# Kernel optimization log

Hardware: AMD Instinct MI355X
Metric: run time of the kernel (lower is better)

Reference implementation:

```python
import jax, jax.numpy as jnp
import numpy as np

B, T, C, K = 8, 2048, 1024, 128

def setup_inputs() -> dict:
    key = jax.random.key(0)
    k1, k2, k3, k4 = jax.random.split(key, 4)
    scale = 0.02
    return {
        "x": jax.random.normal(k1, (B, T, C), dtype=jnp.float32),
        "Wq": jax.random.normal(k2, (C, K), dtype=jnp.float32) * scale,
        "Wk": jax.random.normal(k3, (C, K), dtype=jnp.float32) * scale,
        "Wv": jax.random.normal(k4, (C, K), dtype=jnp.float32) * scale,
    }

def reference(x, Wq, Wk, Wv):
    # Single-head causal self-attention (ModulUwagi.forward)
    q = jnp.einsum('btc,ck->btk', x, Wq)  # [B,T,K]
    k = jnp.einsum('btc,ck->btk', x, Wk)
    v = jnp.einsum('btc,ck->btk', x, Wv)
    hd = q.shape[-1]
    wei = jnp.einsum('btk,bsk->bts', q, k) * (hd ** -0.5)  # [B,T,T]
    causal = jnp.tril(jnp.ones((x.shape[1], x.shape[1]), dtype=bool))
    wei = jnp.where(causal, wei, -jnp.inf)
    wei = jax.nn.softmax(wei, axis=-1)
    out = jnp.einsum('bts,bsk->btk', wei, v)  # [B,T,K]
    return out
```

## Files before the change

kernel.cpp:

```cpp
#include <hip/hip_runtime.h>
#include <cmath>

#define Bn 8
#define Tn 2048
#define Cn 1024
#define Kn 128

typedef __attribute__((ext_vector_type(8))) short short8;
typedef __attribute__((ext_vector_type(4))) float f32x4;
typedef unsigned short u16;
typedef unsigned int u32;

#define NEGINF (-__builtin_huge_valf())

__device__ __forceinline__ u16 f2b(float f) {
    u32 u = __float_as_uint(f);
    u32 r = (u + 0x7FFFu + ((u >> 16) & 1u)) >> 16;
    return (u16)r;
}
__device__ __forceinline__ float b2f(u16 v) {
    u32 u = ((u32)v) << 16;
    return __uint_as_float(u);
}
__device__ __forceinline__ u32 cvtpk(float lo, float hi) {
    u32 r;
    asm("v_cvt_pk_bf16_f32 %0, %1, %2" : "=v"(r) : "v"(lo), "v"(hi));
    return r;
}

__device__ __forceinline__ void load_lds16(const u16* g, u16* l) {
    __builtin_amdgcn_global_load_lds(
        (const __attribute__((address_space(1))) u32*)(g),
        (__attribute__((address_space(3))) u32*)(l), 16, 0, 0);
}

__global__ __launch_bounds__(256)
void prep_kernel(const float* __restrict__ Wq, const float* __restrict__ Wk,
                 const float* __restrict__ Wv, u16* __restrict__ Wt)
{
    int id = blockIdx.x * 256 + threadIdx.x;
    int w   = id >> 15;
    int rem = id & 32767;
    int c   = rem >> 5;
    int n4  = (rem & 31) << 2;
    const float* W = (w == 0) ? Wq : (w == 1) ? Wk : Wv;
    float4 v = *(const float4*)(W + (size_t)c * Kn + n4);
    u16* dst = Wt + (size_t)w * Kn * Cn;
    dst[(size_t)(n4 + 0) * Cn + c] = f2b(v.x);
    dst[(size_t)(n4 + 1) * Cn + c] = f2b(v.y);
    dst[(size_t)(n4 + 2) * Cn + c] = f2b(v.z);
    dst[(size_t)(n4 + 3) * Cn + c] = f2b(v.w);
}

__global__ __launch_bounds__(256)
void proj5_kernel(const float* __restrict__ x, const u16* __restrict__ Wt,
                  u16* __restrict__ qkv)
{
    const int bid = blockIdx.x;
    const int g8  = bid >> 3, xr = bid & 7;
    const int w   = g8 % 3;
    const int rt  = (g8 / 3) * 8 + xr;
    const u16* wtg = Wt + (size_t)w * Kn * Cn;
    u16* outp = qkv + (size_t)w * Bn * Tn * Kn;
    const int row0 = rt * 64;
    const int tid  = threadIdx.x;
    const int lane = tid & 63;
    const int wid  = tid >> 6;
    const int l15  = lane & 15, lh = lane >> 4;
    const int m0 = (wid >> 1) * 32, n0 = (wid & 1) * 64;

    __shared__ u16 lds[24576];

    auto stageW = [&](int kk, int buf) {
        #pragma unroll
        for (int i = 0; i < 4; ++i) {
            int u = tid + i * 256;
            int n = u >> 3, c8 = u & 7;
            load_lds16(wtg + (size_t)n * Cn + kk + ((c8 ^ (n & 7)) << 3),
                       lds + 8192 + buf * 8192 + u * 8);
        }
    };
    auto loadX = [&](int kk, float4* xr4) {
        #pragma unroll
        for (int i = 0; i < 2; ++i) {
            int u = tid + i * 256;
            int r = u >> 3, c8 = u & 7;
            const float* s = x + (size_t)(row0 + r) * Cn + kk + c8 * 8;
            xr4[2 * i]     = *(const float4*)(s);
            xr4[2 * i + 1] = *(const float4*)(s + 4);
        }
    };
    auto writeX = [&](int buf, const float4* xr4) {
        u16* dst = lds + buf * 4096;
        #pragma unroll
        for (int i = 0; i < 2; ++i) {
            int u = tid + i * 256;
            int r = u >> 3, c8 = u & 7;
            uint4 pk;
            pk.x = cvtpk(xr4[2 * i].x,     xr4[2 * i].y);
            pk.y = cvtpk(xr4[2 * i].z,     xr4[2 * i].w);
            pk.z = cvtpk(xr4[2 * i + 1].x, xr4[2 * i + 1].y);
            pk.w = cvtpk(xr4[2 * i + 1].z, xr4[2 * i + 1].w);
            *(uint4*)(dst + r * 64 + ((c8 ^ (r & 7)) << 3)) = pk;
        }
    };

    f32x4 acc[2][4];
    #pragma unroll
    for (int i = 0; i < 2; ++i)
        #pragma unroll
        for (int j = 0; j < 4; ++j) acc[i][j] = (f32x4){0.f, 0.f, 0.f, 0.f};

    auto compute = [&](int buf) {
        const u16* Xb = lds + buf * 4096;
        const u16* Wb = lds + 8192 + buf * 8192;
        #pragma unroll
        for (int kc = 0; kc < 2; ++kc) {
            short8 af[2], bf[4];
            #pragma unroll
            for (int mg = 0; mg < 2; ++mg) {
                int row = m0 + mg * 16 + l15;
                int ch  = (kc * 4 + lh) ^ (row & 7);
                af[mg] = *(const short8*)(Xb + row * 64 + ch * 8);
            }
            #pragma unroll
            for (int ng = 0; ng < 4; ++ng) {
                int n  = n0 + ng * 16 + l15;
                int ch = (kc * 4 + lh) ^ (n & 7);
                bf[ng] = *(const short8*)(Wb + n * 64 + ch * 8);
            }
            #pragma unroll
            for (int mg = 0; mg < 2; ++mg)
                #pragma unroll
                for (int ng = 0; ng < 4; ++ng)
                    acc[mg][ng] = __builtin_amdgcn_mfma_f32_16x16x32_bf16(
                        af[mg], bf[ng], acc[mg][ng], 0, 0, 0);
        }
    };

    float4 xA[4], xB[4];
    loadX(0, xA);
    stageW(0, 0);
    loadX(64, xB);
    writeX(0, xA);
    asm volatile("s_waitcnt vmcnt(4) lgkmcnt(0)" ::: "memory");
    __builtin_amdgcn_sched_barrier(0);
    __builtin_amdgcn_s_barrier();
    __builtin_amdgcn_sched_barrier(0);

    auto step = [&](int t, float4* XW, float4* XL) {
        const int buf = t & 1;
        if (t + 1 < 16) stageW((t + 1) * 64, buf ^ 1);
        if (t + 2 < 16) loadX((t + 2) * 64, XL);
        compute(buf);
        if (t + 1 < 16) writeX(buf ^ 1, XW);
        if (t < 15) {
            if (t < 14)
                asm volatile("s_waitcnt vmcnt(4) lgkmcnt(0)" ::: "memory");
            else
                asm volatile("s_waitcnt vmcnt(0) lgkmcnt(0)" ::: "memory");
            __builtin_amdgcn_sched_barrier(0);
            __builtin_amdgcn_s_barrier();
            __builtin_amdgcn_sched_barrier(0);
        }
    };

    for (int tt = 0; tt < 8; ++tt) {
        step(2 * tt,     xB, xA);
        step(2 * tt + 1, xA, xB);
    }

    #pragma unroll
    for (int mg = 0; mg < 2; ++mg)
        #pragma unroll
        for (int ng = 0; ng < 4; ++ng)
            #pragma unroll
            for (int r = 0; r < 4; ++r) {
                int m = row0 + m0 + mg * 16 + lh * 4 + r;
                int n = n0 + ng * 16 + l15;
                outp[(size_t)m * Kn + n] = f2b(acc[mg][ng][r]);
            }
}

__device__ const int g_job_qi[32] = {0, 1,1, 2,2,2, 3,3,3,3, 4,4,4,4,
                                     5,5,5,5,5, 6,6,6,6,6,6, 7,7,7,7,7,7,7};
__device__ const int g_sup_b[32] = {0, 0,4, 0,4,8, 0,4,8,12, 0,5,10,15,
                                    0,4,9,14,19, 0,4,9,14,18,23, 0,4,9,13,18,22,27};
__device__ const int g_sup_e[32] = {4, 4,8, 4,8,12, 4,8,12,16, 5,10,15,20,
                                    4,9,14,19,24, 4,9,14,18,23,28, 4,9,13,18,22,27,32};

__global__ __launch_bounds__(512, 2)
void attn_kernel(const u16* __restrict__ qg_, const u16* __restrict__ kg_,
                 const u16* __restrict__ vg_, u16* __restrict__ pO,
                 float* __restrict__ pM, float* __restrict__ pL)
{
    const int b   = blockIdx.x;
    const int job = blockIdx.y;
    const int qi  = g_job_qi[job];
    const int sb  = g_sup_b[job], se = g_sup_e[job];

    const u16* qw = qg_ + (size_t)b * Tn * Kn;
    const u16* kw = kg_ + (size_t)b * Tn * Kn;
    const u16* vw = vg_ + (size_t)b * Tn * Kn;

    const int tid  = threadIdx.x;
    const int lane = tid & 63;
    const int wid  = tid >> 6;
    const int l15  = lane & 15, lh = lane >> 4;

    const int q0 = qi * 256 + wid * 32;
    const int qmax_w = q0 + 31;

    __shared__ u16 lds[32768];

    short8 qf[2][4];
    #pragma unroll
    for (int g = 0; g < 2; ++g)
        #pragma unroll
        for (int kc = 0; kc < 4; ++kc)
            qf[g][kc] = *(const short8*)(qw + (size_t)(q0 + g * 16 + l15) * Kn
                                         + kc * 32 + lh * 8);

    f32x4 acc[8][2];
    #pragma unroll
    for (int dt = 0; dt < 8; ++dt)
        #pragma unroll
        for (int g = 0; g < 2; ++g) acc[dt][g] = (f32x4){0.f, 0.f, 0.f, 0.f};
    float m_g[2] = {NEGINF, NEGINF}, l_g[2] = {0.f, 0.f};

    const float scale = 0.08838834764831843f;

    auto stageK = [&](int sup, int buf) {
        const u16* src = kw + (size_t)sup * 64 * Kn;
        u16* dst = lds + buf * 8192;
        #pragma unroll
        for (int i = 0; i < 2; ++i) {
            int u = wid * 128 + i * 64 + lane;
            int row = u >> 4;
            int c16 = (u & 15) ^ (row & 7);
            load_lds16(src + (size_t)row * Kn + c16 * 8,
                       dst + (size_t)(wid * 128 + i * 64) * 8);
        }
    };
    auto loadV = [&](int sup, uint4* vr) {
        const u16* src = vw + (size_t)sup * 64 * Kn;
        #pragma unroll
        for (int r = 0; r < 2; ++r) {
            int s  = tid & 63;
            int u8 = (tid >> 6) + 8 * r;
            vr[r] = *(const uint4*)(src + (size_t)s * Kn + u8 * 8);
        }
    };
    auto writeV = [&](int buf, const uint4* vr) {
        u16* dst = lds + 16384 + buf * 8192;
        #pragma unroll
        for (int r = 0; r < 2; ++r) {
            int s  = tid & 63;
            int u8 = (tid >> 6) + 8 * r;
            const u16* e = (const u16*)&vr[r];
            #pragma unroll
            for (int j = 0; j < 8; ++j) {
                int d = u8 * 8 + j;
                dst[d * 64 + (((s >> 3) ^ j) << 3) + (s & 7)] = e[j];
            }
        }
    };

    uint4 vreg[2];
    stageK(sb, 0);
    loadV(sb, vreg);
    writeV(0, vreg);

    for (int sup = sb; sup < se; ++sup) {
        const int cur = (sup - sb) & 1;
        __syncthreads();
        const bool have_next = (sup + 1 < se);
        if (have_next) {
            stageK(sup + 1, cur ^ 1);
            loadV(sup + 1, vreg);
        }
        if (sup * 64 <= qmax_w) {
            const u16* Kb = lds + cur * 8192;
            const u16* Vb = lds + 16384 + cur * 8192;
            f32x4 sf[4][2];
            #pragma unroll
            for (int mt = 0; mt < 4; ++mt)
                #pragma unroll
                for (int g = 0; g < 2; ++g) sf[mt][g] = (f32x4){0.f,0.f,0.f,0.f};
            #pragma unroll
            for (int kc = 0; kc < 4; ++kc) {
                short8 a[4];
                #pragma unroll
                for (int mt = 0; mt < 4; ++mt) {
                    int row = mt * 16 + l15;
                    int ch  = (kc * 4 + lh) ^ (row & 7);
                    a[mt] = *(const short8*)(Kb + row * 128 + ch * 8);
                }
                #pragma unroll
                for (int mt = 0; mt < 4; ++mt)
                    #pragma unroll
                    for (int g = 0; g < 2; ++g)
                        sf[mt][g] = __builtin_amdgcn_mfma_f32_16x16x32_bf16(
                            a[mt], qf[g][kc], sf[mt][g], 0, 0, 0);
            }
            const int sbase = sup * 64;
            u32 upk[2][4][2];
            float alpha_g[2];
            #pragma unroll
            for (int g = 0; g < 2; ++g) {
                const int qg = q0 + g * 16 + l15;
                float pv[16];
                float pm = NEGINF;
                #pragma unroll
                for (int mt = 0; mt < 4; ++mt)
                    #pragma unroll
                    for (int r = 0; r < 4; ++r) {
                        int sg = sbase + mt * 16 + lh * 4 + r;
                        float vv = sf[mt][g][r] * scale;
                        vv = (sg > qg) ? NEGINF : vv;
                        pv[mt * 4 + r] = vv;
                        pm = fmaxf(pm, vv);
                    }
                pm = fmaxf(pm, __shfl_xor(pm, 16));
                pm = fmaxf(pm, __shfl_xor(pm, 32));
                float mn  = fmaxf(m_g[g], pm);
                float mns = (mn == NEGINF) ? 0.f : mn;
                float al  = __expf(m_g[g] - mns);
                m_g[g] = mn;
                alpha_g[g] = al;
                float ps = 0.f;
                #pragma unroll
                for (int i = 0; i < 16; ++i) { pv[i] = __expf(pv[i] - mns); ps += pv[i]; }
                ps += __shfl_xor(ps, 16);
                ps += __shfl_xor(ps, 32);
                l_g[g] = l_g[g] * al + ps;
                #pragma unroll
                for (int mt = 0; mt < 4; ++mt)
                    #pragma unroll
                    for (int h = 0; h < 2; ++h)
                        upk[g][mt][h] = (u32)f2b(pv[mt * 4 + 2 * h])
                                      | ((u32)f2b(pv[mt * 4 + 2 * h + 1]) << 16);
            }
            #pragma unroll
            for (int dt = 0; dt < 8; ++dt)
                #pragma unroll
                for (int g = 0; g < 2; ++g)
                    acc[dt][g] *= alpha_g[g];
            #pragma unroll
            for (int ks = 0; ks < 2; ++ks) {
                short8 pf[2];
                #pragma unroll
                for (int g = 0; g < 2; ++g) {
                    union { u32 w[4]; short8 v; } uu;
                    #pragma unroll
                    for (int hp = 0; hp < 4; ++hp) {
                        int srcLane = l15 + 16 * ((lh & 1) * 2 + (hp >> 1));
                        u32 vA = __shfl(upk[g][2 * ks][hp & 1], srcLane, 64);
                        u32 vB = __shfl(upk[g][2 * ks + 1][hp & 1], srcLane, 64);
                        uu.w[hp] = (lh < 2) ? vA : vB;
                    }
                    pf[g] = uu.v;
                }
                #pragma unroll
                for (int dt = 0; dt < 8; ++dt) {
                    int d  = dt * 16 + l15;
                    int ch = (ks * 4 + lh) ^ (d & 7);
                    short8 av = *(const short8*)(Vb + d * 64 + ch * 8);
                    #pragma unroll
                    for (int g = 0; g < 2; ++g)
                        acc[dt][g] = __builtin_amdgcn_mfma_f32_16x16x32_bf16(
                            av, pf[g], acc[dt][g], 0, 0, 0);
                }
            }
        }
        if (have_next) writeV(cur ^ 1, vreg);
    }

    const size_t slotrow = ((size_t)b * 32 + job) * 256 + wid * 32;
    #pragma unroll
    for (int g = 0; g < 2; ++g) {
        size_t row = slotrow + g * 16 + l15;
        #pragma unroll
        for (int dt = 0; dt < 8; ++dt) {
            ushort4 o = { f2b(acc[dt][g][0]), f2b(acc[dt][g][1]),
                          f2b(acc[dt][g][2]), f2b(acc[dt][g][3]) };
            *(ushort4*)(pO + row * 128 + dt * 16 + lh * 4) = o;
        }
        if (lh == 0) {
            pM[row] = m_g[g];
            pL[row] = l_g[g];
        }
    }
}

__device__ const int g_cnt[8] = {1, 2, 3, 4, 4, 5, 6, 7};
__device__ const int g_s0[8]  = {0, 1, 3, 6, 10, 14, 19, 25};

__global__ __launch_bounds__(256)
void merge_kernel(const u16* __restrict__ pO, const float* __restrict__ pM,
                  const float* __restrict__ pL, float* __restrict__ out)
{
    const int bid = blockIdx.x;
    const int b   = bid >> 8;
    const int rem = bid & 255;
    const int qi  = rem >> 5;
    const int rg  = rem & 31;
    const int c = g_cnt[qi], s0 = g_s0[qi];
    const int tid = threadIdx.x;
    const int r8 = tid >> 5;
    const int dg = tid & 31;

    const int row = rg * 8 + r8;
    const size_t base = ((size_t)b * 32 + s0) * 256 + row;

    float mv[8];
    float M = NEGINF;
    #pragma unroll
    for (int i = 0; i < 8; ++i)
        if (i < c) { mv[i] = pM[base + (size_t)i * 256]; M = fmaxf(M, mv[i]); }
    float L = 0.f, w[8];
    #pragma unroll
    for (int i = 0; i < 8; ++i)
        if (i < c) {
            float e = __expf(mv[i] - M);
            L += pL[base + (size_t)i * 256] * e;
            w[i] = e;
        }
    const float invL = 1.f / L;

    float4 o = {0.f, 0.f, 0.f, 0.f};
    #pragma unroll
    for (int i = 0; i < 8; ++i)
        if (i < c) {
            ushort4 p = *(const ushort4*)(pO + (base + (size_t)i * 256) * 128 + dg * 4);
            float wi = w[i] * invL;
            o.x = fmaf(wi, b2f(p.x), o.x);
            o.y = fmaf(wi, b2f(p.y), o.y);
            o.z = fmaf(wi, b2f(p.z), o.z);
            o.w = fmaf(wi, b2f(p.w), o.w);
        }
    *(float4*)(out + ((size_t)b * Tn + qi * 256 + row) * Kn + dg * 4) = o;
}

extern "C" void kernel_launch(void* const* d_in, const int* in_sizes, int n_in,
                              void* d_out, int out_size, void* d_ws, size_t ws_size,
                              hipStream_t stream)
{
    const float* x  = (const float*)d_in[0];
    const float* Wq = (const float*)d_in[1];
    const float* Wk = (const float*)d_in[2];
    const float* Wv = (const float*)d_in[3];
    float* out = (float*)d_out;

    u16* ws = (u16*)d_ws;
    const size_t btk = (size_t)Bn * Tn * Kn;
    u16* q  = ws;
    u16* k  = ws + btk;
    u16* v  = ws + 2 * btk;
    u16* Wt = ws + 3 * btk;
    u16* pO = ws + 3 * btk + 393216;
    float* pM = (float*)(pO + (size_t)8388608);
    float* pL = pM + 65536;

    prep_kernel<<<384, 256, 0, stream>>>(Wq, Wk, Wv, Wt);
    proj5_kernel<<<768, 256, 0, stream>>>(x, Wt, ws);
    attn_kernel<<<dim3(Bn, 32), 512, 0, stream>>>(q, k, v, pO, pM, pL);
    merge_kernel<<<2048, 256, 0, stream>>>(pO, pM, pL, out);
}
```

Measured before the change: 67.08 us.

## Halve attention query tile to 128 rows and split into 72 balanced jobs

Attention blocks now cover 128 query rows with 4 waves (256 threads) instead of 256 rows with 8 waves, and the KV range is split into 72 jobs per batch instead of 32. The staging loops are reworked so fewer threads still fill the same K/V LDS tiles, and the merge kernel and workspace offsets are resized to match. The aim is finer load balance and more blocks across CUs. In exchange, each K/V tile is reused by fewer query rows, and there are more partial outputs to write and merge.

```diff
diff --git a/kernel.cpp b/kernel.cpp
--- a/kernel.cpp
+++ b/kernel.cpp
@@ -12,6 +12,7 @@
 typedef unsigned int u32;
 
 #define NEGINF (-__builtin_huge_valf())
+#define NJOBS 72
 
 __device__ __forceinline__ u16 f2b(float f) {
     u32 u = __float_as_uint(f);
@@ -182,14 +183,23 @@
             }
 }
 
-__device__ const int g_job_qi[32] = {0, 1,1, 2,2,2, 3,3,3,3, 4,4,4,4,
-                                     5,5,5,5,5, 6,6,6,6,6,6, 7,7,7,7,7,7,7};
-__device__ const int g_sup_b[32] = {0, 0,4, 0,4,8, 0,4,8,12, 0,5,10,15,
-                                    0,4,9,14,19, 0,4,9,14,18,23, 0,4,9,13,18,22,27};
-__device__ const int g_sup_e[32] = {4, 4,8, 4,8,12, 4,8,12,16, 5,10,15,20,
-                                    4,9,14,19,24, 4,9,14,18,23,28, 4,9,13,18,22,27,32};
-
-__global__ __launch_bounds__(512, 2)
+__device__ const int g_job_qi[NJOBS] = {
+    0, 1, 2,2, 3,3, 4,4,4, 5,5,5, 6,6,6,6, 7,7,7,7,
+    8,8,8,8,8, 9,9,9,9,9, 10,10,10,10,10,10, 11,11,11,11,11,11,
+    12,12,12,12,12,12,12, 13,13,13,13,13,13,13,
+    14,14,14,14,14,14,14,14, 15,15,15,15,15,15,15,15};
+__device__ const int g_sup_b[NJOBS] = {
+    0, 0, 0,3, 0,4, 0,4,7, 0,4,8, 0,4,8,11, 0,4,8,12,
+    0,4,8,12,15, 0,4,8,12,16, 0,4,8,12,16,19, 0,4,8,12,16,20,
+    0,4,8,12,16,20,23, 0,4,8,12,16,20,24,
+    0,4,8,12,16,20,24,27, 0,4,8,12,16,20,24,28};
+__device__ const int g_sup_e[NJOBS] = {
+    2, 4, 3,6, 4,8, 4,7,10, 4,8,12, 4,8,11,14, 4,8,12,16,
+    4,8,12,15,18, 4,8,12,16,20, 4,8,12,16,19,22, 4,8,12,16,20,24,
+    4,8,12,16,20,23,26, 4,8,12,16,20,24,28,
+    4,8,12,16,20,24,27,30, 4,8,12,16,20,24,28,32};
+
+__global__ __launch_bounds__(256, 2)
 void attn_kernel(const u16* __restrict__ qg_, const u16* __restrict__ kg_,
                  const u16* __restrict__ vg_, u16* __restrict__ pO,
                  float* __restrict__ pM, float* __restrict__ pL)
@@ -208,7 +218,7 @@
     const int wid  = tid >> 6;
     const int l15  = lane & 15, lh = lane >> 4;
 
-    const int q0 = qi * 256 + wid * 32;
+    const int q0 = qi * 128 + wid * 32;
     const int qmax_w = q0 + 31;
 
     __shared__ u16 lds[32768];
@@ -234,29 +244,30 @@
         const u16* src = kw + (size_t)sup * 64 * Kn;
         u16* dst = lds + buf * 8192;
         #pragma unroll
-        for (int i = 0; i < 2; ++i) {
-            int u = wid * 128 + i * 64 + lane;
+        for (int i = 0; i < 4; ++i) {
+            int base = wid * 256 + i * 64;
+            int u = base + lane;
             int row = u >> 4;
             int c16 = (u & 15) ^ (row & 7);
             load_lds16(src + (size_t)row * Kn + c16 * 8,
-                       dst + (size_t)(wid * 128 + i * 64) * 8);
+                       dst + (size_t)base * 8);
         }
     };
     auto loadV = [&](int sup, uint4* vr) {
         const u16* src = vw + (size_t)sup * 64 * Kn;
         #pragma unroll
-        for (int r = 0; r < 2; ++r) {
+        for (int r = 0; r < 4; ++r) {
             int s  = tid & 63;
-            int u8 = (tid >> 6) + 8 * r;
+            int u8 = (tid >> 6) + 4 * r;
             vr[r] = *(const uint4*)(src + (size_t)s * Kn + u8 * 8);
         }
     };
     auto writeV = [&](int buf, const uint4* vr) {
         u16* dst = lds + 16384 + buf * 8192;
         #pragma unroll
-        for (int r = 0; r < 2; ++r) {
+        for (int r = 0; r < 4; ++r) {
             int s  = tid & 63;
-            int u8 = (tid >> 6) + 8 * r;
+            int u8 = (tid >> 6) + 4 * r;
             const u16* e = (const u16*)&vr[r];
             #pragma unroll
             for (int j = 0; j < 8; ++j) {
@@ -266,7 +277,7 @@
         }
     };
 
-    uint4 vreg[2];
+    uint4 vreg[4];
     stageK(sb, 0);
     loadV(sb, vreg);
     writeV(0, vreg);
@@ -376,7 +387,7 @@
         if (have_next) writeV(cur ^ 1, vreg);
     }
 
-    const size_t slotrow = ((size_t)b * 32 + job) * 256 + wid * 32;
+    const size_t slotrow = ((size_t)b * NJOBS + job) * 128 + wid * 32;
     #pragma unroll
     for (int g = 0; g < 2; ++g) {
         size_t row = slotrow + g * 16 + l15;
@@ -393,8 +404,8 @@
     }
 }
 
-__device__ const int g_cnt[8] = {1, 2, 3, 4, 4, 5, 6, 7};
-__device__ const int g_s0[8]  = {0, 1, 3, 6, 10, 14, 19, 25};
+__device__ const int g_cnt[16] = {1,1,2,2,3,3,4,4,5,5,6,6,7,7,8,8};
+__device__ const int g_s0[16]  = {0,1,2,4,6,9,12,16,20,25,30,36,42,49,56,64};
 
 __global__ __launch_bounds__(256)
 void merge_kernel(const u16* __restrict__ pO, const float* __restrict__ pM,
@@ -403,27 +414,27 @@
     const int bid = blockIdx.x;
     const int b   = bid >> 8;
     const int rem = bid & 255;
-    const int qi  = rem >> 5;
-    const int rg  = rem & 31;
+    const int qi  = rem >> 4;
+    const int rg  = rem & 15;
     const int c = g_cnt[qi], s0 = g_s0[qi];
     const int tid = threadIdx.x;
     const int r8 = tid >> 5;
     const int dg = tid & 31;
 
     const int row = rg * 8 + r8;
-    const size_t base = ((size_t)b * 32 + s0) * 256 + row;
+    const size_t base = ((size_t)b * NJOBS + s0) * 128 + row;
 
     float mv[8];
     float M = NEGINF;
     #pragma unroll
     for (int i = 0; i < 8; ++i)
-        if (i < c) { mv[i] = pM[base + (size_t)i * 256]; M = fmaxf(M, mv[i]); }
+        if (i < c) { mv[i] = pM[base + (size_t)i * 128]; M = fmaxf(M, mv[i]); }
     float L = 0.f, w[8];
     #pragma unroll
     for (int i = 0; i < 8; ++i)
         if (i < c) {
             float e = __expf(mv[i] - M);
-            L += pL[base + (size_t)i * 256] * e;
+            L += pL[base + (size_t)i * 128] * e;
             w[i] = e;
         }
     const float invL = 1.f / L;
@@ -432,14 +443,14 @@
     #pragma unroll
     for (int i = 0; i < 8; ++i)
         if (i < c) {
-            ushort4 p = *(const ushort4*)(pO + (base + (size_t)i * 256) * 128 + dg * 4);
+            ushort4 p = *(const ushort4*)(pO + (base + (size_t)i * 128) * 128 + dg * 4);
             float wi = w[i] * invL;
             o.x = fmaf(wi, b2f(p.x), o.x);
             o.y = fmaf(wi, b2f(p.y), o.y);
             o.z = fmaf(wi, b2f(p.z), o.z);
             o.w = fmaf(wi, b2f(p.w), o.w);
         }
-    *(float4*)(out + ((size_t)b * Tn + qi * 256 + row) * Kn + dg * 4) = o;
+    *(float4*)(out + ((size_t)b * Tn + qi * 128 + row) * Kn + dg * 4) = o;
 }
 
 extern "C" void kernel_launch(void* const* d_in, const int* in_sizes, int n_in,
@@ -459,11 +470,11 @@
     u16* v  = ws + 2 * btk;
     u16* Wt = ws + 3 * btk;
     u16* pO = ws + 3 * btk + 393216;
-    float* pM = (float*)(pO + (size_t)8388608);
-    float* pL = pM + 65536;
+    float* pM = (float*)(pO + (size_t)9437184);
+    float* pL = pM + 73728;
 
     prep_kernel<<<384, 256, 0, stream>>>(Wq, Wk, Wv, Wt);
     proj5_kernel<<<768, 256, 0, stream>>>(x, Wt, ws);
-    attn_kernel<<<dim3(Bn, 32), 512, 0, stream>>>(q, k, v, pO, pM, pL);
+    attn_kernel<<<dim3(Bn, NJOBS), 256, 0, stream>>>(q, k, v, pO, pM, pL);
     merge_kernel<<<2048, 256, 0, stream>>>(pO, pM, pL, out);
 }
```

Measured after the change: 78.04 us. +16.3%, slower.

## Fuse QKV projections into one block per row tile, load weights directly to registers

Applied to the files above, without the earlier changes.

The projection kernel now computes all three Q/K/V outputs (384 columns) for a 64-row tile in a single 512-thread block, so each x tile is read from global memory and converted to bf16 once instead of three times. Weight fragments are loaded straight from global memory into registers with double buffering, skipping the LDS staging of W. This cuts x traffic roughly threefold and reduces LDS use. The cost is higher register pressure (24 short8 weight fragments per thread), uncoalesced-ish per-lane weight reads that rely on L2, and fewer blocks (256) to spread across the CUs.

```diff
diff --git a/kernel.cpp b/kernel.cpp
--- a/kernel.cpp
+++ b/kernel.cpp
@@ -52,113 +52,94 @@
     dst[(size_t)(n4 + 3) * Cn + c] = f2b(v.w);
 }
 
-__global__ __launch_bounds__(256)
-void proj5_kernel(const float* __restrict__ x, const u16* __restrict__ Wt,
+__global__ __launch_bounds__(512, 2)
+void proj6_kernel(const float* __restrict__ x, const u16* __restrict__ Wt,
                   u16* __restrict__ qkv)
 {
-    const int bid = blockIdx.x;
-    const int g8  = bid >> 3, xr = bid & 7;
-    const int w   = g8 % 3;
-    const int rt  = (g8 / 3) * 8 + xr;
-    const u16* wtg = Wt + (size_t)w * Kn * Cn;
-    u16* outp = qkv + (size_t)w * Bn * Tn * Kn;
+    const int rt   = blockIdx.x;
     const int row0 = rt * 64;
     const int tid  = threadIdx.x;
     const int lane = tid & 63;
     const int wid  = tid >> 6;
     const int l15  = lane & 15, lh = lane >> 4;
-    const int m0 = (wid >> 1) * 32, n0 = (wid & 1) * 64;
-
-    __shared__ u16 lds[24576];
-
-    auto stageW = [&](int kk, int buf) {
-        #pragma unroll
-        for (int i = 0; i < 4; ++i) {
-            int u = tid + i * 256;
-            int n = u >> 3, c8 = u & 7;
-            load_lds16(wtg + (size_t)n * Cn + kk + ((c8 ^ (n & 7)) << 3),
-                       lds + 8192 + buf * 8192 + u * 8);
-        }
-    };
-    auto loadX = [&](int kk, float4* xr4) {
-        #pragma unroll
-        for (int i = 0; i < 2; ++i) {
-            int u = tid + i * 256;
-            int r = u >> 3, c8 = u & 7;
-            const float* s = x + (size_t)(row0 + r) * Cn + kk + c8 * 8;
-            xr4[2 * i]     = *(const float4*)(s);
-            xr4[2 * i + 1] = *(const float4*)(s + 4);
-        }
-    };
-    auto writeX = [&](int buf, const float4* xr4) {
-        u16* dst = lds + buf * 4096;
-        #pragma unroll
-        for (int i = 0; i < 2; ++i) {
-            int u = tid + i * 256;
-            int r = u >> 3, c8 = u & 7;
-            uint4 pk;
-            pk.x = cvtpk(xr4[2 * i].x,     xr4[2 * i].y);
-            pk.y = cvtpk(xr4[2 * i].z,     xr4[2 * i].w);
-            pk.z = cvtpk(xr4[2 * i + 1].x, xr4[2 * i + 1].y);
-            pk.w = cvtpk(xr4[2 * i + 1].z, xr4[2 * i + 1].w);
-            *(uint4*)(dst + r * 64 + ((c8 ^ (r & 7)) << 3)) = pk;
-        }
-    };
-
-    f32x4 acc[2][4];
+    const int wm0 = (wid >> 2) * 32;
+    const int wn0 = (wid & 3) * 96;
+
+    __shared__ u16 xs[8192];
+
+    const u16* wb[6];
+    #pragma unroll
+    for (int ng = 0; ng < 6; ++ng)
+        wb[ng] = Wt + (size_t)(wn0 + ng * 16 + l15) * Cn + lh * 8;
+
+    auto loadW = [&](int kk, short8* wf) {
+        #pragma unroll
+        for (int kc = 0; kc < 2; ++kc)
+            #pragma unroll
+            for (int ng = 0; ng < 6; ++ng)
+                wf[kc * 6 + ng] = *(const short8*)(wb[ng] + kk + kc * 32);
+    };
+    auto loadX = [&](int kk, float4* xr) {
+        int r = tid >> 3, c8 = tid & 7;
+        const float* s = x + (size_t)(row0 + r) * Cn + kk + c8 * 8;
+        xr[0] = *(const float4*)(s);
+        xr[1] = *(const float4*)(s + 4);
+    };
+    auto writeX = [&](int buf, const float4* xr) {
+        int r = tid >> 3, c8 = tid & 7;
+        uint4 pk;
+        pk.x = cvtpk(xr[0].x, xr[0].y);
+        pk.y = cvtpk(xr[0].z, xr[0].w);
+        pk.z = cvtpk(xr[1].x, xr[1].y);
+        pk.w = cvtpk(xr[1].z, xr[1].w);
+        *(uint4*)(xs + buf * 4096 + r * 64 + ((c8 ^ (r & 7)) << 3)) = pk;
+    };
+
+    f32x4 acc[2][6];
     #pragma unroll
     for (int i = 0; i < 2; ++i)
         #pragma unroll
-        for (int j = 0; j < 4; ++j) acc[i][j] = (f32x4){0.f, 0.f, 0.f, 0.f};
-
-    auto compute = [&](int buf) {
-        const u16* Xb = lds + buf * 4096;
-        const u16* Wb = lds + 8192 + buf * 8192;
+        for (int j = 0; j < 6; ++j) acc[i][j] = (f32x4){0.f, 0.f, 0.f, 0.f};
+
+    auto compute = [&](int buf, const short8* wf) {
+        const u16* Xb = xs + buf * 4096;
         #pragma unroll
         for (int kc = 0; kc < 2; ++kc) {
-            short8 af[2], bf[4];
+            short8 af[2];
             #pragma unroll
             for (int mg = 0; mg < 2; ++mg) {
-                int row = m0 + mg * 16 + l15;
+                int row = wm0 + mg * 16 + l15;
                 int ch  = (kc * 4 + lh) ^ (row & 7);
                 af[mg] = *(const short8*)(Xb + row * 64 + ch * 8);
             }
             #pragma unroll
-            for (int ng = 0; ng < 4; ++ng) {
-                int n  = n0 + ng * 16 + l15;
-                int ch = (kc * 4 + lh) ^ (n & 7);
-                bf[ng] = *(const short8*)(Wb + n * 64 + ch * 8);
-            }
-            #pragma unroll
             for (int mg = 0; mg < 2; ++mg)
                 #pragma unroll
-                for (int ng = 0; ng < 4; ++ng)
+                for (int ng = 0; ng < 6; ++ng)
                     acc[mg][ng] = __builtin_amdgcn_mfma_f32_16x16x32_bf16(
-                        af[mg], bf[ng], acc[mg][ng], 0, 0, 0);
-        }
-    };
-
-    float4 xA[4], xB[4];
+                        af[mg], wf[kc * 6 + ng], acc[mg][ng], 0, 0, 0);
+        }
+    };
+
+    short8 wfA[12], wfB[12];
+    float4 xA[2], xB[2];
     loadX(0, xA);
-    stageW(0, 0);
+    loadW(0, wfA);
     loadX(64, xB);
     writeX(0, xA);
-    asm volatile("s_waitcnt vmcnt(4) lgkmcnt(0)" ::: "memory");
+    asm volatile("s_waitcnt lgkmcnt(0)" ::: "memory");
     __builtin_amdgcn_sched_barrier(0);
     __builtin_amdgcn_s_barrier();
     __builtin_amdgcn_sched_barrier(0);
 
-    auto step = [&](int t, float4* XW, float4* XL) {
+    auto step = [&](int t, float4* xW, float4* xL, short8* wfCur, short8* wfNext) {
         const int buf = t & 1;
-        if (t + 1 < 16) stageW((t + 1) * 64, buf ^ 1);
-        if (t + 2 < 16) loadX((t + 2) * 64, XL);
-        compute(buf);
-        if (t + 1 < 16) writeX(buf ^ 1, XW);
+        if (t + 2 < 16) loadX((t + 2) * 64, xL);
+        if (t + 1 < 16) loadW((t + 1) * 64, wfNext);
+        compute(buf, wfCur);
+        if (t + 1 < 16) writeX(buf ^ 1, xW);
         if (t < 15) {
-            if (t < 14)
-                asm volatile("s_waitcnt vmcnt(4) lgkmcnt(0)" ::: "memory");
-            else
-                asm volatile("s_waitcnt vmcnt(0) lgkmcnt(0)" ::: "memory");
+            asm volatile("s_waitcnt lgkmcnt(0)" ::: "memory");
             __builtin_amdgcn_sched_barrier(0);
             __builtin_amdgcn_s_barrier();
             __builtin_amdgcn_sched_barrier(0);
@@ -166,20 +147,24 @@
     };
 
     for (int tt = 0; tt < 8; ++tt) {
-        step(2 * tt,     xB, xA);
-        step(2 * tt + 1, xA, xB);
+        step(2 * tt,     xB, xA, wfA, wfB);
+        step(2 * tt + 1, xA, xB, wfB, wfA);
     }
 
     #pragma unroll
     for (int mg = 0; mg < 2; ++mg)
         #pragma unroll
-        for (int ng = 0; ng < 4; ++ng)
+        for (int ng = 0; ng < 6; ++ng) {
+            int n_glob = wn0 + ng * 16 + l15;
+            int w  = n_glob >> 7;
+            int nl = n_glob & 127;
+            u16* outp = qkv + (size_t)w * Bn * Tn * Kn;
             #pragma unroll
             for (int r = 0; r < 4; ++r) {
-                int m = row0 + m0 + mg * 16 + lh * 4 + r;
-                int n = n0 + ng * 16 + l15;
-                outp[(size_t)m * Kn + n] = f2b(acc[mg][ng][r]);
-            }
+                int m = row0 + wm0 + mg * 16 + lh * 4 + r;
+                outp[(size_t)m * Kn + nl] = f2b(acc[mg][ng][r]);
+            }
+        }
 }
 
 __device__ const int g_job_qi[32] = {0, 1,1, 2,2,2, 3,3,3,3, 4,4,4,4,
@@ -463,7 +448,7 @@
     float* pL = pM + 65536;
 
     prep_kernel<<<384, 256, 0, stream>>>(Wq, Wk, Wv, Wt);
-    proj5_kernel<<<768, 256, 0, stream>>>(x, Wt, ws);
+    proj6_kernel<<<256, 512, 0, stream>>>(x, Wt, ws);
     attn_kernel<<<dim3(Bn, 32), 512, 0, stream>>>(q, k, v, pO, pM, pL);
     merge_kernel<<<2048, 256, 0, stream>>>(pO, pM, pL, out);
 }
```

After: 92.64 us. +38.1%, slower.
